# Kernel tuning notes

Hardware: AMD Instinct MI355X
Metric: run time of the kernel (lower is better)

## Reference

```python
import jax, jax.numpy as jnp
import numpy as np
import math

D_MODEL = 512
D_FF = 4 * D_MODEL
N_EXPERTS = 8
VOCAB = 256
TOL = 0.15          # TeslaHarmonicGate tolerance
HARM = math.pi / 3.0  # harmonic spacing (Tesla 3-6-9 -> pi*k/3 harmonics over [-pi, pi])


def tesla_gate(angle):
    # Snap angle to the nearest harmonic (multiple of pi/3) when within tolerance.
    nearest = jnp.round(angle / HARM) * HARM
    return jnp.where(jnp.abs(angle - nearest) < TOL, nearest, angle)


def setup_inputs() -> dict:
    key = jax.random.key(0)
    ks = jax.random.split(key, 16)
    s = lambda d: 1.0 / np.sqrt(d)
    return {
        "byte_seq": jax.random.randint(ks[0], (4, 2048), 0, VOCAB, dtype=jnp.int32),
        "emb":    jax.random.normal(ks[1], (VOCAB, D_MODEL), jnp.float32) * 0.02,
        "phi_w":  jax.random.normal(ks[2], (D_MODEL, D_MODEL), jnp.float32) * s(D_MODEL),
        "phi_b":  jnp.zeros((D_MODEL,), jnp.float32),
        "amp_w":  jax.random.normal(ks[3], (D_MODEL, D_MODEL), jnp.float32) * s(D_MODEL),
        "amp_b":  jnp.zeros((D_MODEL,), jnp.float32),
        "gate_w": jax.random.normal(ks[4], (D_MODEL, N_EXPERTS), jnp.float32) * s(D_MODEL),
        "gate_b": jnp.zeros((N_EXPERTS,), jnp.float32),
        "w1":     jax.random.normal(ks[5], (N_EXPERTS, D_MODEL, D_FF), jnp.float32) * s(D_MODEL),
        "b1":     jnp.zeros((N_EXPERTS, D_FF), jnp.float32),
        "w2":     jax.random.normal(ks[6], (N_EXPERTS, D_FF, D_MODEL), jnp.float32) * s(D_FF),
        "b2":     jnp.zeros((N_EXPERTS, D_MODEL), jnp.float32),
        "head_w": jax.random.normal(ks[7], (D_MODEL, VOCAB), jnp.float32) * s(D_MODEL),
        "head_b": jnp.zeros((VOCAB,), jnp.float32),
    }


def _toroidal(x, phi_w, phi_b, amp_w, amp_b):
    # x: [B, T, C]; sequential toroidal recurrence over T via lax.scan.
    B, T, C = x.shape
    state0 = jnp.zeros((B, C), x.dtype)

    def step(state, xt):  # xt: [B, C]
        raw_angle = jnp.tanh(xt @ phi_w + phi_b) * jnp.pi
        angle = tesla_gate(raw_angle)
        new_state = jnp.cos(angle) * state - jnp.sin(angle) * (1.0 - state)
        new_state = jnp.clip(new_state, -1.0, 1.0)
        gated = jax.nn.sigmoid(xt @ amp_w + amp_b) * new_state
        return new_state, gated

    final_state, out = jax.lax.scan(step, state0, jnp.swapaxes(x, 0, 1))
    return jnp.swapaxes(out, 0, 1), final_state  # [B,T,C], [B,C]


def _moe(x, gate_w, gate_b, w1, b1, w2, b2):
    # Top-2 softmax routing with renormalized weights; per-expert FFN (GELU).
    B, T, C = x.shape
    xt = x.reshape(B * T, C)                        # [N, C]
    probs = jax.nn.softmax(xt @ gate_w + gate_b)    # [N, E]
    topw, topi = jax.lax.top_k(probs, 2)            # [N, 2]
    topw = topw / jnp.sum(topw, axis=-1, keepdims=True)
    out = jnp.zeros_like(xt)
    for e in range(N_EXPERTS):  # fixed small expert loop
        w_e = jnp.sum(jnp.where(topi == e, topw, 0.0), axis=-1)  # [N]
        h = jax.nn.gelu(xt @ w1[e] + b1[e])
        out = out + w_e[:, None] * (h @ w2[e] + b2[e])
    return out.reshape(B, T, C)


def reference(byte_seq, emb, phi_w, phi_b, amp_w, amp_b, gate_w, gate_b,
              w1, b1, w2, b2, head_w, head_b):
    x = emb[byte_seq]                                  # [B, T, C]
    x, next_state = _toroidal(x, phi_w, phi_b, amp_w, amp_b)
    moe_out = _moe(x, gate_w, gate_b, w1, b1, w2, b2)
    logits = moe_out @ head_w + head_b                 # [B, T, 256]
    return logits, next_state
```

## Files before the change

### kernel.cpp

```cpp
#include <hip/hip_runtime.h>
#include <hip/hip_fp16.h>
#include <math.h>


#define PI_F 3.14159265358979323846f
#define HARM_F 1.04719755119659774615f
#define INV_HARM_F 0.95492965855137201461f
#define TOL_F 0.15f

typedef float f32x16 __attribute__((ext_vector_type(16)));
typedef __bf16 bf16x8 __attribute__((ext_vector_type(8)));
typedef unsigned int u32x4 __attribute__((ext_vector_type(4)));
typedef unsigned int u32x2 __attribute__((ext_vector_type(2)));

__device__ __forceinline__ float gelu_tanh(float x) {
  float x3 = x * x * x;
  return 0.5f * x * (1.f + tanhf(0.79788456080286535588f * (x + 0.044715f * x3)));
}
__device__ __forceinline__ unsigned short f2bf(float x) {
  unsigned u = __float_as_uint(x);
  unsigned r = (u + 0x7FFFu + ((u >> 16) & 1u)) >> 16;
  return (unsigned short)r;
}
__device__ __forceinline__ float bflo(unsigned u) { return __uint_as_float(u << 16); }
__device__ __forceinline__ float bfhi(unsigned u) { return __uint_as_float(u & 0xFFFF0000u); }
__device__ __forceinline__ bf16x8 ld_frag(const void* p) {
  u32x4 v = *(const u32x4*)p;
  return __builtin_bit_cast(bf16x8, v);
}

__device__ __forceinline__ float tanh_fast(float z) {
  float zc = fminf(10.f, fmaxf(-10.f, z));
  float e2 = __expf(zc + zc);
  return (e2 - 1.f) / (e2 + 1.f);
}
__device__ __forceinline__ float sigmoid_fast(float z) {
  return 1.f / (1.f + __expf(-z));
}
__device__ __forceinline__ void sincos_poly(float a, float* sn, float* cs) {
  float q = rintf(a * 0.63661977236758134f);
  int iq = (int)q;
  float t = fmaf(-q, 1.57079637050628662f, a);
  t = fmaf(q, 4.37113883e-8f, t);
  float t2 = t * t;
  float sp = t * fmaf(t2, fmaf(t2, fmaf(t2, -1.9515296e-4f, 8.3321609e-3f),
                               -1.6666654e-1f), 1.f);
  float cp = fmaf(t2 * t2,
                  fmaf(t2, fmaf(t2, 2.4433158e-5f, -1.3887316e-3f), 4.1666646e-2f),
                  fmaf(t2, -0.5f, 1.f));
  int m = iq & 3;
  bool swap = (m & 1) != 0;
  float ss = swap ? cp : sp;
  float cc = swap ? sp : cp;
  *sn = (m & 2) ? -ss : ss;
  *cs = ((m + 1) & 2) ? -cc : cc;
}

__global__ void k_embed(const int* __restrict__ seq, const float* __restrict__ emb,
                        float* __restrict__ X) {
  int i = blockIdx.x * 256 + threadIdx.x;
  int n = i >> 7, c4 = i & 127;
  int tok = seq[n];
  ((float4*)X)[(size_t)n * 128 + c4] = ((const float4*)emb)[(size_t)tok * 128 + c4];
}

__global__ __launch_bounds__(256) void k_pack_b(const float* __restrict__ src, int ld,
                                                size_t srcE, unsigned short* __restrict__ dst,
                                                size_t dstE, int fragKtot) {
  __shared__ float Ls[512 * 33];
  int nb = blockIdx.x, kseg = blockIdx.y, e = blockIdx.z;
  const float* s = src + (size_t)e * srcE + (size_t)kseg * 512 * ld + nb * 32;
  unsigned short* d = dst + (size_t)e * dstE + ((size_t)(nb * fragKtot + kseg * 32)) * 512;
  int tid = threadIdx.x;
#pragma unroll
  for (int q = 0; q < 16; ++q) {
    int i = tid + q * 256;
    int row = i >> 3, c4 = i & 7;
    float4 v = *(const float4*)(s + (size_t)row * ld + c4 * 4);
    Ls[row * 33 + c4 * 4 + 0] = v.x;
    Ls[row * 33 + c4 * 4 + 1] = v.y;
    Ls[row * 33 + c4 * 4 + 2] = v.z;
    Ls[row * 33 + c4 * 4 + 3] = v.w;
  }
  __syncthreads();
#pragma unroll
  for (int q = 0; q < 8; ++q) {
    int i = tid + q * 256;
    int ks = i >> 6, l = i & 63;
    int col = l & 31, kb = (l >> 5) * 8 + ks * 16;
    u32x4 o;
    o.x = (unsigned)f2bf(Ls[(kb + 0) * 33 + col]) | ((unsigned)f2bf(Ls[(kb + 1) * 33 + col]) << 16);
    o.y = (unsigned)f2bf(Ls[(kb + 2) * 33 + col]) | ((unsigned)f2bf(Ls[(kb + 3) * 33 + col]) << 16);
    o.z = (unsigned)f2bf(Ls[(kb + 4) * 33 + col]) | ((unsigned)f2bf(Ls[(kb + 5) * 33 + col]) << 16);
    o.w = (unsigned)f2bf(Ls[(kb + 6) * 33 + col]) | ((unsigned)f2bf(Ls[(kb + 7) * 33 + col]) << 16);
    *(u32x4*)(d + (size_t)ks * 512 + l * 8) = o;
  }
}

__global__ __launch_bounds__(256, 2) void k_phi(const float* __restrict__ A,
                                                const float* __restrict__ phiW,
                                                const float* __restrict__ phiB,
                                                const float* __restrict__ ampW,
                                                const float* __restrict__ ampB,
                                                float* __restrict__ cosO,
                                                float* __restrict__ sinO,
                                                float* __restrict__ sigO) {
  __shared__ float As[2][16 * 132];
  __shared__ float Bs[2][16 * 132];
  int tid = threadIdx.x;
  int tx = tid & 15, ty = tid >> 4;
  int bm = blockIdx.x * 128;
  int by = blockIdx.y;
  const float* Bsrc = (by < 4) ? phiW : ampW;
  const float* bias = (by < 4) ? phiB : ampB;
  int cb = (by & 3) * 128;
  float acc[8][8];
#pragma unroll
  for (int r = 0; r < 8; ++r)
#pragma unroll
    for (int c = 0; c < 8; ++c) acc[r][c] = 0.f;

#define STAGE_PHI(BUF, KT)                                                     \
  {                                                                            \
    _Pragma("unroll") for (int s = 0; s < 2; ++s) {                            \
      int i = tid + s * 256;                                                   \
      int row = i >> 2, kq = i & 3;                                            \
      float4 v = *(const float4*)(A + (size_t)(bm + row) * 512 + (KT)*16 + kq * 4); \
      As[BUF][(kq * 4 + 0) * 132 + row] = v.x;                                 \
      As[BUF][(kq * 4 + 1) * 132 + row] = v.y;                                 \
      As[BUF][(kq * 4 + 2) * 132 + row] = v.z;                                 \
      As[BUF][(kq * 4 + 3) * 132 + row] = v.w;                                 \
    }                                                                          \
    _Pragma("unroll") for (int s = 0; s < 2; ++s) {                            \
      int i = tid + s * 256;                                                   \
      int kk = i >> 5, g = i & 31;                                             \
      float4 v = *(const float4*)(Bsrc + (size_t)((KT)*16 + kk) * 512 + cb + g * 4); \
      *(float4*)(&Bs[BUF][kk * 132 + g * 4]) = v;                              \
    }                                                                          \
  }

  STAGE_PHI(0, 0);
  for (int kt = 0; kt < 32; ++kt) {
    __syncthreads();
    if (kt + 1 < 32) {
      if ((kt & 1) == 0) STAGE_PHI(1, kt + 1) else STAGE_PHI(0, kt + 1)
    }
    const float* Ab = As[kt & 1];
    const float* Bb = Bs[kt & 1];
#pragma unroll
    for (int kk = 0; kk < 16; ++kk) {
      float4 a0 = *(const float4*)(&Ab[kk * 132 + ty * 4]);
      float4 a1 = *(const float4*)(&Ab[kk * 132 + 64 + ty * 4]);
      float4 b0 = *(const float4*)(&Bb[kk * 132 + tx * 4]);
      float4 b1 = *(const float4*)(&Bb[kk * 132 + 64 + tx * 4]);
      float ar[8] = {a0.x, a0.y, a0.z, a0.w, a1.x, a1.y, a1.z, a1.w};
      float br[8] = {b0.x, b0.y, b0.z, b0.w, b1.x, b1.y, b1.z, b1.w};
#pragma unroll
      for (int r = 0; r < 8; ++r)
#pragma unroll
        for (int c = 0; c < 8; ++c) acc[r][c] = fmaf(ar[r], br[c], acc[r][c]);
    }
  }
#pragma unroll
  for (int rh = 0; rh < 2; ++rh) {
#pragma unroll
    for (int rr = 0; rr < 4; ++rr) {
      int r = rh * 4 + rr;
      int m = bm + rh * 64 + ty * 4 + rr;
      if (by < 4) {
#pragma unroll
        for (int ch = 0; ch < 2; ++ch) {
          float o0[4], o1[4];
#pragma unroll
          for (int cc = 0; cc < 4; ++cc) {
            float z = acc[r][ch * 4 + cc] + bias[cb + ch * 64 + tx * 4 + cc];
            float a = tanh_fast(z) * PI_F;
            float nr = rintf(a * INV_HARM_F) * HARM_F;
            if (fabsf(a - nr) < TOL_F) a = nr;
            float sn, cs;
            sincos_poly(a, &sn, &cs);
            o0[cc] = cs;
            o1[cc] = sn;
          }
          float* cp = cosO + (size_t)m * 512 + cb + ch * 64 + tx * 4;
          float* sp = sinO + (size_t)m * 512 + cb + ch * 64 + tx * 4;
          *(float4*)cp = make_float4(o0[0], o0[1], o0[2], o0[3]);
          *(float4*)sp = make_float4(o1[0], o1[1], o1[2], o1[3]);
        }
      } else {
#pragma unroll
        for (int ch = 0; ch < 2; ++ch) {
          float o0[4];
#pragma unroll
          for (int cc = 0; cc < 4; ++cc) {
            float z = acc[r][ch * 4 + cc] + bias[cb + ch * 64 + tx * 4 + cc];
            o0[cc] = sigmoid_fast(z);
          }
          float* gp = sigO + (size_t)m * 512 + cb + ch * 64 + tx * 4;
          *(float4*)gp = make_float4(o0[0], o0[1], o0[2], o0[3]);
        }
      }
    }
  }
}

__global__ __launch_bounds__(256, 1) void k_scan(const float* __restrict__ cosb,
                                                 const float* __restrict__ sinb,
                                                 const float* __restrict__ sigb,
                                                 float* __restrict__ xmoe,
                                                 float* __restrict__ nstate) {
  __shared__ float lds[2][3][64 * 64];
  int tid = threadIdx.x;
  int wv = tid >> 6, l = tid & 63;
  int b = blockIdx.x >> 3;
  int c0 = (blockIdx.x & 7) << 6;
  size_t base = ((size_t)b * 2048) * 512 + c0;

#define SCAN_STAGE(SRC, K, BUF)                                                \
  {                                                                            \
    float4 tmp[16];                                                            \
    size_t sb = base + ((size_t)(K) * 64 + tq) * 512 + cq * 4;                 \
    _Pragma("unroll") for (int t4 = 0; t4 < 16; ++t4)                          \
      tmp[t4] = *(const float4*)((SRC) + sb + (size_t)t4 * 4 * 512);           \
    _Pragma("unroll") for (int t4 = 0; t4 < 16; ++t4)                          \
      *(float4*)(&lds[BUF][wv - 1][(t4 * 4 + tq) * 64 + cq * 4]) = tmp[t4];    \
  }

  if (wv > 0) {
    const float* src = (wv == 1) ? cosb : (wv == 2) ? sinb : sigb;
    int tq = l >> 4, cq = l & 15;
    SCAN_STAGE(src, 0, 0);
    __syncthreads();
    for (int k = 0; k < 32; ++k) {
      if (k + 1 < 32) {
        if (((k + 1) & 1) == 0) SCAN_STAGE(src, k + 1, 0)
        else                    SCAN_STAGE(src, k + 1, 1)
      }
      __syncthreads();
    }
  } else {
    __syncthreads();
    float state = 0.f;
    for (int k = 0; k < 32; ++k) {
      const float* bufC = &lds[k & 1][0][0];
      const float* bufS = &lds[k & 1][1][0];
      const float* bufG = &lds[k & 1][2][0];
      size_t outb = base + (size_t)k * 64 * 512 + l;
#pragma unroll
      for (int tt = 0; tt < 64; ++tt) {
        float pc = bufC[tt * 64 + l];
        float ps = bufS[tt * 64 + l];
        float pg = bufG[tt * 64 + l];
        float st = fmaf(pc + ps, state, -ps);
        st = fminf(1.f, fmaxf(-1.f, st));
        state = st;
        xmoe[outb + (size_t)tt * 512] = pg * st;
      }
      __syncthreads();
    }
    nstate[(size_t)b * 512 + c0 + l] = state;
  }
}

__global__ __launch_bounds__(256) void k_gate(const float* __restrict__ xmoe,
                                              const float* __restrict__ gw_g,
                                              const float* __restrict__ gb,
                                              int* __restrict__ e01p,
                                              unsigned* __restrict__ w01p) {
  __shared__ float gw[4096];
  int tid = threadIdx.x;
  for (int i = tid; i < 4096; i += 256) gw[i] = gw_g[i];
  __syncthreads();
  int tok = blockIdx.x * 32 + (tid >> 3);
  int e = tid & 7;
  float acc = gb[e];
  const float4* xr = (const float4*)(xmoe + (size_t)tok * 512);
  for (int k4 = 0; k4 < 128; ++k4) {
    float4 x = xr[k4];
    acc += x.x * gw[(k4 * 4 + 0) * 8 + e];
    acc += x.y * gw[(k4 * 4 + 1) * 8 + e];
    acc += x.z * gw[(k4 * 4 + 2) * 8 + e];
    acc += x.w * gw[(k4 * 4 + 3) * 8 + e];
  }
  float m = acc;
  m = fmaxf(m, __shfl_xor(m, 1));
  m = fmaxf(m, __shfl_xor(m, 2));
  m = fmaxf(m, __shfl_xor(m, 4));
  float p = expf(acc - m);
  float ss = p;
  ss += __shfl_xor(ss, 1); ss += __shfl_xor(ss, 2); ss += __shfl_xor(ss, 4);
  p /= ss;
  float v1 = p; int i1 = e;
  {
    float ov; int oi;
    ov = __shfl_xor(v1, 1); oi = __shfl_xor(i1, 1);
    if (ov > v1 || (ov == v1 && oi < i1)) { v1 = ov; i1 = oi; }
    ov = __shfl_xor(v1, 2); oi = __shfl_xor(i1, 2);
    if (ov > v1 || (ov == v1 && oi < i1)) { v1 = ov; i1 = oi; }
    ov = __shfl_xor(v1, 4); oi = __shfl_xor(i1, 4);
    if (ov > v1 || (ov == v1 && oi < i1)) { v1 = ov; i1 = oi; }
  }
  float v2 = (e == i1) ? -1.f : p; int i2 = e;
  {
    float ov; int oi;
    ov = __shfl_xor(v2, 1); oi = __shfl_xor(i2, 1);
    if (ov > v2 || (ov == v2 && oi < i2)) { v2 = ov; i2 = oi; }
    ov = __shfl_xor(v2, 2); oi = __shfl_xor(i2, 2);
    if (ov > v2 || (ov == v2 && oi < i2)) { v2 = ov; i2 = oi; }
    ov = __shfl_xor(v2, 4); oi = __shfl_xor(i2, 4);
    if (ov > v2 || (ov == v2 && oi < i2)) { v2 = ov; i2 = oi; }
  }
  if (e == 0) {
    float s2 = v1 + v2;
    __half h1 = __float2half(v1 / s2), h2 = __float2half(v2 / s2);
    e01p[tok] = i1 | (i2 << 8);
    w01p[tok] = (unsigned)__half_as_ushort(h1) | ((unsigned)__half_as_ushort(h2) << 16);
  }
}

__global__ void k_build(const int* __restrict__ e01p, const unsigned* __restrict__ w01p,
                        int* __restrict__ list, float* __restrict__ wlist,
                        int* __restrict__ counts, int* __restrict__ eoff,
                        int* __restrict__ tokpos, int* __restrict__ tmap) {
  __shared__ int cnt[8], cur[8];
  int tid = threadIdx.x, lane = tid & 63;
  if (tid < 8) cnt[tid] = 0;
  __syncthreads();
  for (int i = tid; i < 16384; i += 256) {
    int tok = i >> 1, j = i & 1;
    int ee = (e01p[tok] >> (8 * j)) & 255;
#pragma unroll
    for (int x = 0; x < 8; ++x) {
      unsigned long long m = __ballot(ee == x);
      if (m != 0ull && lane == (__ffsll((long long)m) - 1)) atomicAdd(&cnt[x], __popcll(m));
    }
  }
  __syncthreads();
  if (tid == 0) {
    int s = 0;
#pragma unroll
    for (int x = 0; x < 8; ++x) {
      cur[x] = s; eoff[x] = s; counts[x] = cnt[x]; s += cnt[x];
    }
  }
  __syncthreads();
  for (int i = tid; i < 272; i += 256) tmap[i] = -1;
  __syncthreads();
  if (tid == 0) {
    int ntiles = 0, tstart[8];
#pragma unroll
    for (int e = 0; e < 8; ++e) { tstart[e] = ntiles; ntiles += (cnt[e] + 95) / 96; }
    int q = ntiles >> 3, r = ntiles & 7;
    for (int e = 0; e < 8; ++e) {
      int nt = (cnt[e] + 95) / 96;
      for (int t = 0; t < nt; ++t) {
        int k = tstart[e] + t;
        int c, o;
        if (k < r * (q + 1)) { c = k / (q + 1); o = k - c * (q + 1); }
        else { int k2 = k - r * (q + 1); c = r + k2 / q; o = k2 - (k2 / q) * q; }
        tmap[8 * o + c] = (e << 16) | t;
      }
    }
  }
  __syncthreads();
  for (int i = tid; i < 16384; i += 256) {
    int tok = i >> 1, j = i & 1;
    int ee = (e01p[tok] >> (8 * j)) & 255;
    unsigned wp = w01p[tok];
    unsigned short us = (unsigned short)(j ? (wp >> 16) : (wp & 0xFFFFu));
    float w = __half2float(__ushort_as_half(us));
    int pos = 0;
#pragma unroll
    for (int x = 0; x < 8; ++x) {
      unsigned long long m = __ballot(ee == x);
      if (m == 0ull) continue;
      int leader = __ffsll((long long)m) - 1;
      int bb = 0;
      if (lane == leader) bb = atomicAdd(&cur[x], __popcll(m));
      bb = __shfl(bb, leader);
      if (ee == x) pos = bb + __popcll(m & ((1ull << lane) - 1ull));
    }
    list[pos] = tok;
    wlist[pos] = w;
    tokpos[i] = pos;
  }
}

#define HS_OFF 98304

__global__ __launch_bounds__(512, 2) void k_ffn(
    const float* __restrict__ xmoe, const int* __restrict__ list,
    const float* __restrict__ wlist, const int* __restrict__ counts,
    const int* __restrict__ eoff, const int* __restrict__ tmap,
    const unsigned short* __restrict__ W1Pk, const float* __restrict__ b1g,
    const unsigned short* __restrict__ W2Pk, const float* __restrict__ b2g,
    unsigned short* __restrict__ Yb) {
  int mp = tmap[blockIdx.x];
  if (mp < 0) return;
  int e = mp >> 16, tile = mp & 0xFFFF;
  int cnt = counts[e];
  int base = eoff[e] + tile * 96;
  int valid = cnt - tile * 96;
  if (valid > 96) valid = 96;
  __shared__ __align__(16) char smem[147456];
  __shared__ int toks[96];
  __shared__ float wts[96];
  int tid = threadIdx.x;
  int w = tid >> 6, l = tid & 63;
  int l31 = l & 31, hi = l >> 5;
  if (tid < 96) {
    int idx = tile * 96 + tid;
    bool v = idx < cnt;
    toks[tid] = list[eoff[e] + (v ? idx : 0)];
    wts[tid] = v ? wlist[eoff[e] + idx] : 0.f;
  }
  __syncthreads();
#pragma unroll
  for (int s = 0; s < 12; ++s) {
    int sl = s * 512 + tid;
    int ent = sl >> 6, ll = sl & 63;
    int ks = ent / 3, t3 = ent - ks * 3;
    int tok = toks[t3 * 32 + (ll & 31)];
    const float* src = xmoe + (size_t)tok * 512 + ks * 16 + (ll >> 5) * 8;
    float4 v0 = *(const float4*)src;
    float4 v1 = *(const float4*)(src + 4);
    u32x4 u;
    u.x = (unsigned)f2bf(v0.x) | ((unsigned)f2bf(v0.y) << 16);
    u.y = (unsigned)f2bf(v0.z) | ((unsigned)f2bf(v0.w) << 16);
    u.z = (unsigned)f2bf(v1.x) | ((unsigned)f2bf(v1.y) << 16);
    u.w = (unsigned)f2bf(v1.z) | ((unsigned)f2bf(v1.w) << 16);
    *(u32x4*)(smem + ent * 1024 + ll * 16) = u;
  }
  f32x16 acc00, acc01, acc02, acc10, acc11, acc12;
#pragma unroll
  for (int i = 0; i < 16; ++i) {
    acc00[i] = 0.f; acc01[i] = 0.f; acc02[i] = 0.f;
    acc10[i] = 0.f; acc11[i] = 0.f; acc12[i] = 0.f;
  }
  __syncthreads();

  const size_t dstE1 = (size_t)64 * 32 * 512;
  const size_t dstE2 = (size_t)16 * 128 * 512;
  for (int it = 0; it < 8; ++it) {
    f32x16 z0, z1, z2;
#pragma unroll
    for (int i = 0; i < 16; ++i) { z0[i] = 0.f; z1[i] = 0.f; z2[i] = 0.f; }
    const unsigned short* w1p =
        W1Pk + (size_t)e * dstE1 + ((size_t)(it * 8 + w) * 32) * 512 + l * 8;
#pragma unroll 8
    for (int ks = 0; ks < 32; ++ks) {
      bf16x8 a = *(const bf16x8*)(w1p + (size_t)ks * 512);
      bf16x8 b0 = ld_frag(smem + (ks * 3 + 0) * 1024 + l * 16);
      bf16x8 b1 = ld_frag(smem + (ks * 3 + 1) * 1024 + l * 16);
      bf16x8 b2 = ld_frag(smem + (ks * 3 + 2) * 1024 + l * 16);
      z0 = __builtin_amdgcn_mfma_f32_32x32x16_bf16(a, b0, z0, 0, 0, 0);
      z1 = __builtin_amdgcn_mfma_f32_32x32x16_bf16(a, b1, z1, 0, 0, 0);
      z2 = __builtin_amdgcn_mfma_f32_32x32x16_bf16(a, b2, z2, 0, 0, 0);
    }
#define GELU_STORE(Z, T3)                                                       \
  {                                                                             \
    _Pragma("unroll") for (int rq = 0; rq < 4; ++rq) {                          \
      int fb = w * 32 + 8 * rq + 4 * hi;                                        \
      float4 bv = *(const float4*)(b1g + e * 2048 + it * 256 + fb);             \
      float g0 = gelu_tanh(Z[4 * rq + 0] + bv.x);                               \
      float g1 = gelu_tanh(Z[4 * rq + 1] + bv.y);                               \
      float g2 = gelu_tanh(Z[4 * rq + 2] + bv.z);                               \
      float g3 = gelu_tanh(Z[4 * rq + 3] + bv.w);                               \
      u32x2 p;                                                                  \
      p.x = (unsigned)f2bf(g0) | ((unsigned)f2bf(g1) << 16);                    \
      p.y = (unsigned)f2bf(g2) | ((unsigned)f2bf(g3) << 16);                    \
      int ent = (w * 2 + (rq >> 1)) * 3 + (T3);                                 \
      int lanep = l31 + 32 * (rq & 1);                                          \
      *(u32x2*)(smem + HS_OFF + ent * 1024 + lanep * 16 + hi * 8) = p;          \
    }                                                                           \
  }
    GELU_STORE(z0, 0)
    GELU_STORE(z1, 1)
    GELU_STORE(z2, 2)
    __syncthreads();
    const unsigned short* w2a =
        W2Pk + (size_t)e * dstE2 + ((size_t)(w * 2) * 128 + it * 16) * 512 + l * 8;
    const unsigned short* w2b = w2a + (size_t)128 * 512;
#pragma unroll 8
    for (int fs = 0; fs < 16; ++fs) {
      bf16x8 a0 = *(const bf16x8*)(w2a + (size_t)fs * 512);
      bf16x8 a1 = *(const bf16x8*)(w2b + (size_t)fs * 512);
      bf16x8 h0 = ld_frag(smem + HS_OFF + (fs * 3 + 0) * 1024 + l * 16);
      bf16x8 h1 = ld_frag(smem + HS_OFF + (fs * 3 + 1) * 1024 + l * 16);
      bf16x8 h2 = ld_frag(smem + HS_OFF + (fs * 3 + 2) * 1024 + l * 16);
      acc00 = __builtin_amdgcn_mfma_f32_32x32x16_bf16(a0, h0, acc00, 0, 0, 0);
      acc01 = __builtin_amdgcn_mfma_f32_32x32x16_bf16(a0, h1, acc01, 0, 0, 0);
      acc02 = __builtin_amdgcn_mfma_f32_32x32x16_bf16(a0, h2, acc02, 0, 0, 0);
      acc10 = __builtin_amdgcn_mfma_f32_32x32x16_bf16(a1, h0, acc10, 0, 0, 0);
      acc11 = __builtin_amdgcn_mfma_f32_32x32x16_bf16(a1, h1, acc11, 0, 0, 0);
      acc12 = __builtin_amdgcn_mfma_f32_32x32x16_bf16(a1, h2, acc12, 0, 0, 0);
    }
    __syncthreads();
  }
#define EPI_STORE(ACC, JC, T3)                                                  \
  {                                                                             \
    _Pragma("unroll") for (int rq = 0; rq < 4; ++rq) {                          \
      int c0 = (w * 2 + (JC)) * 32 + 8 * rq + 4 * hi;                           \
      float4 b2v = *(const float4*)(b2g + e * 512 + c0);                        \
      int tok = (T3)*32 + l31;                                                  \
      float wt = wts[tok];                                                      \
      u32x2 p;                                                                  \
      p.x = (unsigned)f2bf((ACC[4 * rq + 0] + b2v.x) * wt) |                    \
            ((unsigned)f2bf((ACC[4 * rq + 1] + b2v.y) * wt) << 16);             \
      p.y = (unsigned)f2bf((ACC[4 * rq + 2] + b2v.z) * wt) |                    \
            ((unsigned)f2bf((ACC[4 * rq + 3] + b2v.w) * wt) << 16);             \
      *(u32x2*)(smem + tok * 1024 + ((c0 * 2) ^ ((tok & 7) << 4))) = p;         \
    }                                                                           \
  }
  EPI_STORE(acc00, 0, 0)
  EPI_STORE(acc01, 0, 1)
  EPI_STORE(acc02, 0, 2)
  EPI_STORE(acc10, 1, 0)
  EPI_STORE(acc11, 1, 1)
  EPI_STORE(acc12, 1, 2)
  __syncthreads();
#pragma unroll
  for (int s = 0; s < 12; ++s) {
    int i = tid + s * 512;
    int row = i >> 6, g = i & 63;
    if (row < valid) {
      u32x4 v = *(u32x4*)(smem + row * 1024 + ((g * 16) ^ ((row & 7) << 4)));
      *(u32x4*)(Yb + (size_t)(base + row) * 512 + g * 8) = v;
    }
  }
}

__global__ __launch_bounds__(256) void k_head(const unsigned short* __restrict__ Yb,
                                              const int* __restrict__ tokpos,
                                              const unsigned short* __restrict__ headPk,
                                              const float* __restrict__ headB,
                                              float* __restrict__ out) {
  __shared__ __align__(16) char As[16384];
  __shared__ int tp[256];
  int tid = threadIdx.x;
  int w = tid >> 6, l = tid & 63;
  int l31 = l & 31, hi = l >> 5;
  int mg = w & 1, ng = w >> 1;
  int bm = blockIdx.x * 128, by = blockIdx.y;
  tp[tid] = tokpos[bm * 2 + tid];
  f32x16 acc00, acc01, acc10, acc11;
#pragma unroll
  for (int i = 0; i < 16; ++i) { acc00[i] = 0.f; acc01[i] = 0.f; acc10[i] = 0.f; acc11[i] = 0.f; }
  int nblk0 = by * 4 + ng * 2;
  __syncthreads();
  for (int kb = 0; kb < 8; ++kb) {
#pragma unroll
    for (int s = 0; s < 4; ++s) {
      int i = tid + s * 256;
      int row = i >> 3, g = i & 7;
      int p1 = tp[row * 2], p2 = tp[row * 2 + 1];
      u32x4 va = *(const u32x4*)(Yb + (size_t)p1 * 512 + kb * 64 + g * 8);
      u32x4 vb = *(const u32x4*)(Yb + (size_t)p2 * 512 + kb * 64 + g * 8);
      u32x4 o;
      o.x = (unsigned)f2bf(bflo(va.x) + bflo(vb.x)) | ((unsigned)f2bf(bfhi(va.x) + bfhi(vb.x)) << 16);
      o.y = (unsigned)f2bf(bflo(va.y) + bflo(vb.y)) | ((unsigned)f2bf(bfhi(va.y) + bfhi(vb.y)) << 16);
      o.z = (unsigned)f2bf(bflo(va.z) + bflo(vb.z)) | ((unsigned)f2bf(bfhi(va.z) + bfhi(vb.z)) << 16);
      o.w = (unsigned)f2bf(bflo(va.w) + bflo(vb.w)) | ((unsigned)f2bf(bfhi(va.w) + bfhi(vb.w)) << 16);
      *(u32x4*)(As + row * 128 + ((g * 16) ^ ((row & 7) << 4))) = o;
    }
    __syncthreads();
#pragma unroll
    for (int ks = 0; ks < 4; ++ks) {
      int r0 = mg * 64 + l31, r1 = r0 + 32;
      int kbyte = ks * 32 + hi * 16;
      bf16x8 a0 = ld_frag(As + r0 * 128 + (kbyte ^ ((r0 & 7) << 4)));
      bf16x8 a1 = ld_frag(As + r1 * 128 + (kbyte ^ ((r1 & 7) << 4)));
      const unsigned short* hp = headPk + ((size_t)nblk0 * 32 + kb * 4 + ks) * 512 + l * 8;
      bf16x8 b0 = *(const bf16x8*)hp;
      bf16x8 b1 = *(const bf16x8*)(hp + 32 * 512);
      acc00 = __builtin_amdgcn_mfma_f32_32x32x16_bf16(a0, b0, acc00, 0, 0, 0);
      acc01 = __builtin_amdgcn_mfma_f32_32x32x16_bf16(a0, b1, acc01, 0, 0, 0);
      acc10 = __builtin_amdgcn_mfma_f32_32x32x16_bf16(a1, b0, acc10, 0, 0, 0);
      acc11 = __builtin_amdgcn_mfma_f32_32x32x16_bf16(a1, b1, acc11, 0, 0, 0);
    }
    __syncthreads();
  }
#pragma unroll
  for (int mf = 0; mf < 2; ++mf) {
#pragma unroll
    for (int nf = 0; nf < 2; ++nf) {
      int nc = by * 128 + ng * 64 + nf * 32 + l31;
      float hb = headB[nc];
#pragma unroll
      for (int r = 0; r < 16; ++r) {
        int m = bm + mg * 64 + mf * 32 + (r & 3) + 8 * (r >> 2) + 4 * hi;
        float v;
        if (mf == 0) v = (nf == 0) ? acc00[r] : acc01[r];
        else         v = (nf == 0) ? acc10[r] : acc11[r];
        out[(size_t)m * 256 + nc] = v + hb;
      }
    }
  }
}

extern "C" void kernel_launch(void* const* d_in, const int* in_sizes, int n_in,
                              void* d_out, int out_size, void* d_ws, size_t ws_size,
                              hipStream_t stream) {
  (void)in_sizes; (void)n_in; (void)out_size; (void)ws_size;
  const int* seq     = (const int*)d_in[0];
  const float* emb   = (const float*)d_in[1];
  const float* phi_w = (const float*)d_in[2];
  const float* phi_b = (const float*)d_in[3];
  const float* amp_w = (const float*)d_in[4];
  const float* amp_b = (const float*)d_in[5];
  const float* gate_w = (const float*)d_in[6];
  const float* gate_b = (const float*)d_in[7];
  const float* w1 = (const float*)d_in[8];
  const float* b1 = (const float*)d_in[9];
  const float* w2 = (const float*)d_in[10];
  const float* b2 = (const float*)d_in[11];
  const float* head_w = (const float*)d_in[12];
  const float* head_b = (const float*)d_in[13];
  float* out = (float*)d_out;

  char* ws = (char*)d_ws;
  const size_t BUF = 16777216;
  float* X    = (float*)(ws);
  float* COSb = (float*)(ws + BUF);
  float* SINb = (float*)(ws + 2 * BUF);
  float* SIGb = (float*)(ws + 3 * BUF);
  unsigned short* Yb   = (unsigned short*)COSb;
  unsigned short* W1Pk = (unsigned short*)SINb;
  unsigned short* W2Pk = (unsigned short*)SIGb;
  char* sm = ws + 4 * BUF;
  int*      e01p   = (int*)(sm);
  unsigned* w01p   = (unsigned*)(sm + 32768);
  int*      list   = (int*)(sm + 65536);
  float*    wlist  = (float*)(sm + 131072);
  int*      tokpos = (int*)(sm + 196608);
  int*      counts = (int*)(sm + 262144);
  int*      eoff   = (int*)(sm + 262144 + 64);
  unsigned short* headPk = (unsigned short*)(sm + 266240);
  int*      tmap   = (int*)(sm + 266240 + 262144);

  k_embed<<<4096, 256, 0, stream>>>(seq, emb, X);
  k_pack_b<<<dim3(8, 1, 1), 256, 0, stream>>>(head_w, 256, 0, headPk, 0, 32);
  k_phi<<<dim3(64, 8), 256, 0, stream>>>(X, phi_w, phi_b, amp_w, amp_b, COSb, SINb, SIGb);
  k_scan<<<32, 256, 0, stream>>>(COSb, SINb, SIGb, X, out + 2097152);
  k_pack_b<<<dim3(64, 1, 8), 256, 0, stream>>>(w1, 2048, (size_t)512 * 2048, W1Pk,
                                               (size_t)64 * 32 * 512, 32);
  k_pack_b<<<dim3(16, 4, 8), 256, 0, stream>>>(w2, 512, (size_t)2048 * 512, W2Pk,
                                               (size_t)16 * 128 * 512, 128);
  k_gate<<<256, 256, 0, stream>>>(X, gate_w, gate_b, e01p, w01p);
  k_build<<<1, 256, 0, stream>>>(e01p, w01p, list, wlist, counts, eoff, tokpos, tmap);
  k_ffn<<<192, 512, 0, stream>>>(X, list, wlist, counts, eoff, tmap,
                                 W1Pk, b1, W2Pk, b2, Yb);
  k_head<<<dim3(64, 2), 256, 0, stream>>>(Yb, tokpos, headPk, head_b, out);
}
```

Before: 450.6 us.

## Run phi/amp projection on bf16x3 split MFMA with embed packing hi/lo fragments

The embedding kernel now writes tokens as pre-packed bf16 hi/lo MFMA fragments. The phi/amp projection replaces its fp32 FMA tiling with 32x32x16 bf16 MFMAs using a three-term split (hi*hi, lo*hi, hi*lo) to keep near-fp32 accuracy. Weights are converted and split into LDS per k-step. The aim is to move the dominant projection GEMM off scalar FMA onto matrix cores. The cost is extra conversion work and scattered per-element epilogue stores. GELU also switches to the fast tanh.

```diff
diff --git a/kernel.cpp b/kernel.cpp
--- a/kernel.cpp
+++ b/kernel.cpp
@@ -13,22 +13,17 @@
 typedef unsigned int u32x4 __attribute__((ext_vector_type(4)));
 typedef unsigned int u32x2 __attribute__((ext_vector_type(2)));
 
-__device__ __forceinline__ float gelu_tanh(float x) {
-  float x3 = x * x * x;
-  return 0.5f * x * (1.f + tanhf(0.79788456080286535588f * (x + 0.044715f * x3)));
-}
+__device__ __forceinline__ float bflo(unsigned u) { return __uint_as_float(u << 16); }
+__device__ __forceinline__ float bfhi(unsigned u) { return __uint_as_float(u & 0xFFFF0000u); }
 __device__ __forceinline__ unsigned short f2bf(float x) {
   unsigned u = __float_as_uint(x);
   unsigned r = (u + 0x7FFFu + ((u >> 16) & 1u)) >> 16;
   return (unsigned short)r;
 }
-__device__ __forceinline__ float bflo(unsigned u) { return __uint_as_float(u << 16); }
-__device__ __forceinline__ float bfhi(unsigned u) { return __uint_as_float(u & 0xFFFF0000u); }
 __device__ __forceinline__ bf16x8 ld_frag(const void* p) {
   u32x4 v = *(const u32x4*)p;
   return __builtin_bit_cast(bf16x8, v);
 }
-
 __device__ __forceinline__ float tanh_fast(float z) {
   float zc = fminf(10.f, fmaxf(-10.f, z));
   float e2 = __expf(zc + zc);
@@ -36,6 +31,11 @@
 }
 __device__ __forceinline__ float sigmoid_fast(float z) {
   return 1.f / (1.f + __expf(-z));
+}
+__device__ __forceinline__ float gelu_tanh(float x) {
+  float x3 = x * x * x;
+  float t = 0.79788456080286535588f * (x + 0.044715f * x3);
+  return 0.5f * x * (1.f + tanh_fast(t));
 }
 __device__ __forceinline__ void sincos_poly(float a, float* sn, float* cs) {
   float q = rintf(a * 0.63661977236758134f);
@@ -56,12 +56,31 @@
   *cs = ((m + 1) & 2) ? -cc : cc;
 }
 
-__global__ void k_embed(const int* __restrict__ seq, const float* __restrict__ emb,
-                        float* __restrict__ X) {
-  int i = blockIdx.x * 256 + threadIdx.x;
-  int n = i >> 7, c4 = i & 127;
-  int tok = seq[n];
-  ((float4*)X)[(size_t)n * 128 + c4] = ((const float4*)emb)[(size_t)tok * 128 + c4];
+__global__ void k_embed2(const int* __restrict__ seq, const float* __restrict__ emb,
+                         unsigned short* __restrict__ XhiP,
+                         unsigned short* __restrict__ XloP) {
+  int gid = blockIdx.x * 256 + threadIdx.x;
+  int ent = gid >> 6, l = gid & 63;
+  int tb = ent >> 5, ks = ent & 31;
+  int tok = tb * 32 + (l & 31);
+  int k0 = ks * 16 + (l >> 5) * 8;
+  const float* src = emb + (size_t)seq[tok] * 512 + k0;
+  float4 v0 = *(const float4*)src;
+  float4 v1 = *(const float4*)(src + 4);
+  float vv[8] = {v0.x, v0.y, v0.z, v0.w, v1.x, v1.y, v1.z, v1.w};
+  unsigned h[8], lo[8];
+#pragma unroll
+  for (int j = 0; j < 8; ++j) {
+    h[j] = f2bf(vv[j]);
+    lo[j] = f2bf(vv[j] - bflo(h[j]));
+  }
+  u32x4 H, L;
+  H.x = h[0] | (h[1] << 16);  H.y = h[2] | (h[3] << 16);
+  H.z = h[4] | (h[5] << 16);  H.w = h[6] | (h[7] << 16);
+  L.x = lo[0] | (lo[1] << 16); L.y = lo[2] | (lo[3] << 16);
+  L.z = lo[4] | (lo[5] << 16); L.w = lo[6] | (lo[7] << 16);
+  *(u32x4*)(XhiP + (size_t)ent * 512 + l * 8) = H;
+  *(u32x4*)(XloP + (size_t)ent * 512 + l * 8) = L;
 }
 
 __global__ __launch_bounds__(256) void k_pack_b(const float* __restrict__ src, int ld,
@@ -97,111 +116,100 @@
   }
 }
 
-__global__ __launch_bounds__(256, 2) void k_phi(const float* __restrict__ A,
-                                                const float* __restrict__ phiW,
-                                                const float* __restrict__ phiB,
-                                                const float* __restrict__ ampW,
-                                                const float* __restrict__ ampB,
-                                                float* __restrict__ cosO,
-                                                float* __restrict__ sinO,
-                                                float* __restrict__ sigO) {
-  __shared__ float As[2][16 * 132];
-  __shared__ float Bs[2][16 * 132];
+__global__ __launch_bounds__(256, 3) void k_phi(
+    const unsigned short* __restrict__ XhiP, const unsigned short* __restrict__ XloP,
+    const float* __restrict__ phiW, const float* __restrict__ phiB,
+    const float* __restrict__ ampW, const float* __restrict__ ampB,
+    float* __restrict__ cosO, float* __restrict__ sinO, float* __restrict__ sigO) {
+  __shared__ __align__(16) char wlds[2][8][1024];
   int tid = threadIdx.x;
-  int tx = tid & 15, ty = tid >> 4;
-  int bm = blockIdx.x * 128;
+  int w = tid >> 6, l = tid & 63;
+  int l31 = l & 31, hi = l >> 5;
   int by = blockIdx.y;
   const float* Bsrc = (by < 4) ? phiW : ampW;
   const float* bias = (by < 4) ? phiB : ampB;
   int cb = (by & 3) * 128;
-  float acc[8][8];
-#pragma unroll
-  for (int r = 0; r < 8; ++r)
-#pragma unroll
-    for (int c = 0; c < 8; ++c) acc[r][c] = 0.f;
-
-#define STAGE_PHI(BUF, KT)                                                     \
-  {                                                                            \
-    _Pragma("unroll") for (int s = 0; s < 2; ++s) {                            \
-      int i = tid + s * 256;                                                   \
-      int row = i >> 2, kq = i & 3;                                            \
-      float4 v = *(const float4*)(A + (size_t)(bm + row) * 512 + (KT)*16 + kq * 4); \
-      As[BUF][(kq * 4 + 0) * 132 + row] = v.x;                                 \
-      As[BUF][(kq * 4 + 1) * 132 + row] = v.y;                                 \
-      As[BUF][(kq * 4 + 2) * 132 + row] = v.z;                                 \
-      As[BUF][(kq * 4 + 3) * 132 + row] = v.w;                                 \
-    }                                                                          \
-    _Pragma("unroll") for (int s = 0; s < 2; ++s) {                            \
-      int i = tid + s * 256;                                                   \
-      int kk = i >> 5, g = i & 31;                                             \
-      float4 v = *(const float4*)(Bsrc + (size_t)((KT)*16 + kk) * 512 + cb + g * 4); \
-      *(float4*)(&Bs[BUF][kk * 132 + g * 4]) = v;                              \
-    }                                                                          \
-  }
-
-  STAGE_PHI(0, 0);
-  for (int kt = 0; kt < 32; ++kt) {
+
+#define STAGE_W(KS, BUF)                                                        \
+  {                                                                             \
+    const float* wsrc = Bsrc + (size_t)((KS)*16 + hi * 8) * 512 + cb + w * 32 + l31; \
+    float v0 = wsrc[0],    v1 = wsrc[512],  v2 = wsrc[1024], v3 = wsrc[1536];   \
+    float v4 = wsrc[2048], v5 = wsrc[2560], v6 = wsrc[3072], v7 = wsrc[3584];   \
+    unsigned h0 = f2bf(v0), h1 = f2bf(v1), h2 = f2bf(v2), h3 = f2bf(v3);        \
+    unsigned h4 = f2bf(v4), h5 = f2bf(v5), h6 = f2bf(v6), h7 = f2bf(v7);        \
+    u32x4 H, L;                                                                 \
+    H.x = h0 | (h1 << 16); H.y = h2 | (h3 << 16);                               \
+    H.z = h4 | (h5 << 16); H.w = h6 | (h7 << 16);                               \
+    L.x = (unsigned)f2bf(v0 - bflo(h0)) | ((unsigned)f2bf(v1 - bflo(h1)) << 16); \
+    L.y = (unsigned)f2bf(v2 - bflo(h2)) | ((unsigned)f2bf(v3 - bflo(h3)) << 16); \
+    L.z = (unsigned)f2bf(v4 - bflo(h4)) | ((unsigned)f2bf(v5 - bflo(h5)) << 16); \
+    L.w = (unsigned)f2bf(v6 - bflo(h6)) | ((unsigned)f2bf(v7 - bflo(h7)) << 16); \
+    *(u32x4*)(&wlds[BUF][w * 2 + 0][l * 16]) = H;                               \
+    *(u32x4*)(&wlds[BUF][w * 2 + 1][l * 16]) = L;                               \
+  }
+
+  int tb = blockIdx.x * 4 + w;
+  const unsigned short* xh_base = XhiP + ((size_t)tb * 32) * 512 + l * 8;
+  const unsigned short* xl_base = XloP + ((size_t)tb * 32) * 512 + l * 8;
+  f32x16 a0, a1, a2, a3;
+#pragma unroll
+  for (int i = 0; i < 16; ++i) { a0[i] = 0.f; a1[i] = 0.f; a2[i] = 0.f; a3[i] = 0.f; }
+
+  STAGE_W(0, 0);
+  for (int ks = 0; ks < 32; ++ks) {
     __syncthreads();
-    if (kt + 1 < 32) {
-      if ((kt & 1) == 0) STAGE_PHI(1, kt + 1) else STAGE_PHI(0, kt + 1)
-    }
-    const float* Ab = As[kt & 1];
-    const float* Bb = Bs[kt & 1];
-#pragma unroll
-    for (int kk = 0; kk < 16; ++kk) {
-      float4 a0 = *(const float4*)(&Ab[kk * 132 + ty * 4]);
-      float4 a1 = *(const float4*)(&Ab[kk * 132 + 64 + ty * 4]);
-      float4 b0 = *(const float4*)(&Bb[kk * 132 + tx * 4]);
-      float4 b1 = *(const float4*)(&Bb[kk * 132 + 64 + tx * 4]);
-      float ar[8] = {a0.x, a0.y, a0.z, a0.w, a1.x, a1.y, a1.z, a1.w};
-      float br[8] = {b0.x, b0.y, b0.z, b0.w, b1.x, b1.y, b1.z, b1.w};
-#pragma unroll
-      for (int r = 0; r < 8; ++r)
-#pragma unroll
-        for (int c = 0; c < 8; ++c) acc[r][c] = fmaf(ar[r], br[c], acc[r][c]);
-    }
-  }
-#pragma unroll
-  for (int rh = 0; rh < 2; ++rh) {
-#pragma unroll
-    for (int rr = 0; rr < 4; ++rr) {
-      int r = rh * 4 + rr;
-      int m = bm + rh * 64 + ty * 4 + rr;
-      if (by < 4) {
-#pragma unroll
-        for (int ch = 0; ch < 2; ++ch) {
-          float o0[4], o1[4];
-#pragma unroll
-          for (int cc = 0; cc < 4; ++cc) {
-            float z = acc[r][ch * 4 + cc] + bias[cb + ch * 64 + tx * 4 + cc];
-            float a = tanh_fast(z) * PI_F;
-            float nr = rintf(a * INV_HARM_F) * HARM_F;
-            if (fabsf(a - nr) < TOL_F) a = nr;
-            float sn, cs;
-            sincos_poly(a, &sn, &cs);
-            o0[cc] = cs;
-            o1[cc] = sn;
-          }
-          float* cp = cosO + (size_t)m * 512 + cb + ch * 64 + tx * 4;
-          float* sp = sinO + (size_t)m * 512 + cb + ch * 64 + tx * 4;
-          *(float4*)cp = make_float4(o0[0], o0[1], o0[2], o0[3]);
-          *(float4*)sp = make_float4(o1[0], o1[1], o1[2], o1[3]);
-        }
-      } else {
-#pragma unroll
-        for (int ch = 0; ch < 2; ++ch) {
-          float o0[4];
-#pragma unroll
-          for (int cc = 0; cc < 4; ++cc) {
-            float z = acc[r][ch * 4 + cc] + bias[cb + ch * 64 + tx * 4 + cc];
-            o0[cc] = sigmoid_fast(z);
-          }
-          float* gp = sigO + (size_t)m * 512 + cb + ch * 64 + tx * 4;
-          *(float4*)gp = make_float4(o0[0], o0[1], o0[2], o0[3]);
-        }
-      }
-    }
-  }
+    if (ks + 1 < 32) {
+      if (((ks + 1) & 1) == 0) STAGE_W(ks + 1, 0) else STAGE_W(ks + 1, 1)
+    }
+    bf16x8 xh = *(const bf16x8*)(xh_base + (size_t)ks * 512);
+    bf16x8 xl = *(const bf16x8*)(xl_base + (size_t)ks * 512);
+    const char (*wb)[1024] = wlds[ks & 1];
+    bf16x8 wh0 = ld_frag(&wb[0][l * 16]), wl0 = ld_frag(&wb[1][l * 16]);
+    bf16x8 wh1 = ld_frag(&wb[2][l * 16]), wl1 = ld_frag(&wb[3][l * 16]);
+    bf16x8 wh2 = ld_frag(&wb[4][l * 16]), wl2 = ld_frag(&wb[5][l * 16]);
+    bf16x8 wh3 = ld_frag(&wb[6][l * 16]), wl3 = ld_frag(&wb[7][l * 16]);
+    a0 = __builtin_amdgcn_mfma_f32_32x32x16_bf16(xh, wh0, a0, 0, 0, 0);
+    a1 = __builtin_amdgcn_mfma_f32_32x32x16_bf16(xh, wh1, a1, 0, 0, 0);
+    a2 = __builtin_amdgcn_mfma_f32_32x32x16_bf16(xh, wh2, a2, 0, 0, 0);
+    a3 = __builtin_amdgcn_mfma_f32_32x32x16_bf16(xh, wh3, a3, 0, 0, 0);
+    a0 = __builtin_amdgcn_mfma_f32_32x32x16_bf16(xl, wh0, a0, 0, 0, 0);
+    a1 = __builtin_amdgcn_mfma_f32_32x32x16_bf16(xl, wh1, a1, 0, 0, 0);
+    a2 = __builtin_amdgcn_mfma_f32_32x32x16_bf16(xl, wh2, a2, 0, 0, 0);
+    a3 = __builtin_amdgcn_mfma_f32_32x32x16_bf16(xl, wh3, a3, 0, 0, 0);
+    a0 = __builtin_amdgcn_mfma_f32_32x32x16_bf16(xh, wl0, a0, 0, 0, 0);
+    a1 = __builtin_amdgcn_mfma_f32_32x32x16_bf16(xh, wl1, a1, 0, 0, 0);
+    a2 = __builtin_amdgcn_mfma_f32_32x32x16_bf16(xh, wl2, a2, 0, 0, 0);
+    a3 = __builtin_amdgcn_mfma_f32_32x32x16_bf16(xh, wl3, a3, 0, 0, 0);
+  }
+
+  int tokBase = blockIdx.x * 128 + w * 32;
+#define PHI_EPI(ACC, NB)                                                        \
+  {                                                                             \
+    int c = cb + (NB)*32 + l31;                                                 \
+    float bs = bias[c];                                                         \
+    if (by < 4) {                                                               \
+      _Pragma("unroll") for (int r = 0; r < 16; ++r) {                          \
+        int tok = tokBase + (r & 3) + 8 * (r >> 2) + 4 * hi;                    \
+        float z = ACC[r] + bs;                                                  \
+        float a = tanh_fast(z) * PI_F;                                          \
+        float nr = rintf(a * INV_HARM_F) * HARM_F;                              \
+        if (fabsf(a - nr) < TOL_F) a = nr;                                      \
+        float sn, cs;                                                           \
+        sincos_poly(a, &sn, &cs);                                               \
+        cosO[(size_t)tok * 512 + c] = cs;                                       \
+        sinO[(size_t)tok * 512 + c] = sn;                                       \
+      }                                                                         \
+    } else {                                                                    \
+      _Pragma("unroll") for (int r = 0; r < 16; ++r) {                          \
+        int tok = tokBase + (r & 3) + 8 * (r >> 2) + 4 * hi;                    \
+        sigO[(size_t)tok * 512 + c] = sigmoid_fast(ACC[r] + bs);                \
+      }                                                                         \
+    }                                                                           \
+  }
+  PHI_EPI(a0, 0)
+  PHI_EPI(a1, 1)
+  PHI_EPI(a2, 2)
+  PHI_EPI(a3, 3)
 }
 
 __global__ __launch_bounds__(256, 1) void k_scan(const float* __restrict__ cosb,
@@ -624,6 +632,8 @@
   float* COSb = (float*)(ws + BUF);
   float* SINb = (float*)(ws + 2 * BUF);
   float* SIGb = (float*)(ws + 3 * BUF);
+  unsigned short* XhiP = (unsigned short*)X;
+  unsigned short* XloP = XhiP + (size_t)8192 * 512;
   unsigned short* Yb   = (unsigned short*)COSb;
   unsigned short* W1Pk = (unsigned short*)SINb;
   unsigned short* W2Pk = (unsigned short*)SIGb;
@@ -638,9 +648,10 @@
   unsigned short* headPk = (unsigned short*)(sm + 266240);
   int*      tmap   = (int*)(sm + 266240 + 262144);
 
-  k_embed<<<4096, 256, 0, stream>>>(seq, emb, X);
+  k_embed2<<<2048, 256, 0, stream>>>(seq, emb, XhiP, XloP);
   k_pack_b<<<dim3(8, 1, 1), 256, 0, stream>>>(head_w, 256, 0, headPk, 0, 32);
-  k_phi<<<dim3(64, 8), 256, 0, stream>>>(X, phi_w, phi_b, amp_w, amp_b, COSb, SINb, SIGb);
+  k_phi<<<dim3(64, 8), 256, 0, stream>>>(XhiP, XloP, phi_w, phi_b, amp_w, amp_b,
+                                         COSb, SINb, SIGb);
   k_scan<<<32, 256, 0, stream>>>(COSb, SINb, SIGb, X, out + 2097152);
   k_pack_b<<<dim3(64, 1, 8), 256, 0, stream>>>(w1, 2048, (size_t)512 * 2048, W1Pk,
                                                (size_t)64 * 32 * 512, 32);
```

After: 393.5 us (median of 2 runs). 12.7% less time.
